# Kernel tuning notes

Measured on AMD Instinct MI355X. Metric: run time of the kernel, lower is better.

The kernel has to match this reference:

```python
import jax, jax.numpy as jnp
import numpy as np

LEAKY_ALPHA = 0.2  # LeakyReLU negative slope from init arg `alpha`


def setup_inputs() -> dict:
    key = jax.random.key(0)
    k1, k2, k3, k4 = jax.random.split(key, 4)
    B, N, Fin, Fout = 8, 2048, 256, 256
    h = jax.random.normal(k1, (B, N, Fin), dtype=jnp.float32)
    adj = jax.random.randint(k2, (N, N), 0, 2, dtype=jnp.int32)
    W = jax.random.normal(k3, (Fin, Fout), dtype=jnp.float32) * (1.414 * (6.0 / (Fin + Fout)) ** 0.5)
    a = jax.random.normal(k4, (2 * Fout, 1), dtype=jnp.float32) * (1.414 * (6.0 / (2 * Fout + 1)) ** 0.5)
    return {"h": h, "adj": adj, "W": W, "a": a}


def reference(h, adj, W, a):
    # h: (B, N, Fin), adj: (N, N) int {0,1}, W: (Fin, Fout), a: (2*Fout, 1)
    Fout = W.shape[1]
    Wh = jnp.einsum('bnf,fo->bno', h, W)            # (B, N, Fout)
    a1 = a[:Fout, 0]                                  # attends to target node i
    a2 = a[Fout:, 0]                                  # attends to source node j
    # a^T [Wh_i || Wh_j] == (Wh_i . a1) + (Wh_j . a2); LeakyReLU applied after, as in original
    s_i = Wh @ a1                                     # (B, N)
    s_j = Wh @ a2                                     # (B, N)
    e = jax.nn.leaky_relu(s_i[:, :, None] + s_j[:, None, :], negative_slope=LEAKY_ALPHA)  # (B, N, N)
    N = Wh.shape[1]
    mask = (adj > 0) | jnp.eye(N, dtype=bool)         # adjacency + self-loops
    e = jnp.where(mask[None, :, :], e, -jnp.inf)
    attention = jax.nn.softmax(e, axis=-1)            # dropout is identity in eval
    attention = jnp.nan_to_num(attention, nan=0.0)
    h_prime = jnp.einsum('bij,bjo->bio', attention, Wh)  # (B, N, Fout)
    return jax.nn.elu(h_prime)                        # concat=True -> ELU
```

## Files before the change

### kernel.cpp

```cpp
#include <hip/hip_runtime.h>

typedef unsigned short u16;
typedef unsigned int   u32;
typedef unsigned long long u64;

typedef __bf16 bf16x8 __attribute__((ext_vector_type(8)));
typedef float  f32x4  __attribute__((ext_vector_type(4)));

#define MFMA_BF16(a,b,c) __builtin_amdgcn_mfma_f32_16x16x32_bf16((a),(b),(c),0,0,0)

__device__ __forceinline__ float bf2f(u16 u) {
    return __uint_as_float(((u32)u) << 16);
}
__device__ __forceinline__ u16 f2bf(float x) {
    u32 u = __float_as_uint(x);
    u += 0x7fffu + ((u >> 16) & 1u);
    return (u16)(u >> 16);
}
__device__ __forceinline__ float ldany(const void* p, size_t i, int f32) {
    return f32 ? ((const float*)p)[i] : bf2f(((const u16*)p)[i]);
}
__device__ __forceinline__ int detect_f32(const u32* hw) {
    u32 w = hw[threadIdx.x & 63];
    int e = (w >> 23) & 0xFF;
    u64 m = __ballot(e >= 64 && e <= 190);
    return __popcll(m) >= 32 ? 1 : 0;
}

__global__ __launch_bounds__(256) void kprep(const void* __restrict__ w, const void* __restrict__ a,
                                             const int* __restrict__ adj,
                                             u16* __restrict__ wt, float* __restrict__ wa1,
                                             float* __restrict__ wa2, u64* __restrict__ mb64,
                                             int* __restrict__ cnt, const u32* __restrict__ hw) {
    __shared__ float s1[4], s2[4];
    int bid = blockIdx.x, t = threadIdx.x;
    int wid = t >> 6, lane = t & 63;
    if (bid < 256) {
        if (bid == 0 && t < 8) cnt[t] = 0;
        int f32 = detect_f32(hw);
        int k = bid, o = t;
        float wv = ldany(w, (size_t)k * 256 + o, f32);
        wt[o * 256 + k] = f2bf(wv);
        float p1 = wv * ldany(a, o, f32);
        float p2 = wv * ldany(a, 256 + o, f32);
        for (int d = 32; d; d >>= 1) { p1 += __shfl_down(p1, d); p2 += __shfl_down(p2, d); }
        if (lane == 0) { s1[wid] = p1; s2[wid] = p2; }
        __syncthreads();
        if (o == 0) { wa1[k] = s1[0] + s1[1] + s1[2] + s1[3]; wa2[k] = s2[0] + s2[1] + s2[2] + s2[3]; }
    } else {
        int w2 = (bid - 256) * 4 + wid;
        int4 v[2]; int rowv[2], jbv[2];
        #pragma unroll
        for (int s = 0; s < 2; s++) {
            int task = w2 * 2 + s;
            int row = task >> 3, jb = (task & 7) * 256;
            rowv[s] = row; jbv[s] = jb;
            v[s] = *(const int4*)(adj + (size_t)row * 2048 + jb + lane * 4);
        }
        #pragma unroll
        for (int s = 0; s < 2; s++) {
            int row = rowv[s], jb = jbv[s];
            int j0 = jb + lane * 4;
            u32 nib = (u32)(v[s].x > 0 || j0     == row)
                    | ((u32)(v[s].y > 0 || j0 + 1 == row) << 1)
                    | ((u32)(v[s].z > 0 || j0 + 2 == row) << 2)
                    | ((u32)(v[s].w > 0 || j0 + 3 == row) << 3);
            u32 sh = 4 * (lane & 7);
            u32 lo = (lane & 8) ? 0u : (nib << sh);
            u32 hi = (lane & 8) ? (nib << sh) : 0u;
            #pragma unroll
            for (int d = 1; d <= 8; d <<= 1) {
                lo |= __shfl_xor(lo, d);
                hi |= __shfl_xor(hi, d);
            }
            if ((lane & 15) == 0)
                mb64[(size_t)row * 32 + (jb >> 6) + (lane >> 4)] =
                    (u64)lo | ((u64)hi << 32);
        }
    }
}

struct __align__(16) K2LDS {
    u16 At[64 * 68];
    union { u16 Bt[256 * 68]; u16 Ct[256 * 68]; };
    float wa1s[256], wa2s[256];
    float s1[64], s2[64];
};
__global__ __launch_bounds__(1024, 4) void k2(const void* __restrict__ h, const u16* __restrict__ wt,
                                              const float* __restrict__ wa1, const float* __restrict__ wa2,
                                              u16* __restrict__ whbt,
                                              float* __restrict__ sig, float* __restrict__ sjg) {
    __shared__ K2LDS L;
    int f32 = detect_f32((const u32*)h);
    int m0 = blockIdx.x * 64;
    int b  = m0 >> 11;
    int n0 = m0 & 2047;
    int t = threadIdx.x;
    int wid = t >> 6, lane = t & 63, ln = lane & 15, qd = lane >> 4;

    if (t < 256) { L.wa1s[t] = wa1[t]; L.wa2s[t] = wa2[t]; }
    if (t < 64) { L.s1[t] = 0.f; L.s2[t] = 0.f; }
    __syncthreads();

    float a1 = 0.f, a2 = 0.f;
    f32x4 acc[4];
    for (int mi = 0; mi < 4; mi++) acc[mi] = (f32x4){0.f, 0.f, 0.f, 0.f};

    for (int c = 0; c < 4; c++) {
        int k0c = c * 64;
        if (t < 512) {
            int r = t >> 3, s = t & 7;
            float xv[8]; u16 uv[8];
            if (f32) {
                const float* src = (const float*)h + (size_t)(m0 + r) * 256 + k0c + s * 8;
                f32x4 x0 = *(const f32x4*)src;
                f32x4 x1 = *(const f32x4*)(src + 4);
                #pragma unroll
                for (int q = 0; q < 4; q++) { xv[q] = x0[q]; xv[4 + q] = x1[q]; }
                #pragma unroll
                for (int q = 0; q < 8; q++) uv[q] = f2bf(xv[q]);
            } else {
                const u16* src = (const u16*)h + (size_t)(m0 + r) * 256 + k0c + s * 8;
                *(uint4*)uv = *(const uint4*)src;
                #pragma unroll
                for (int q = 0; q < 8; q++) xv[q] = bf2f(uv[q]);
            }
            *(uint4*)&L.At[r * 68 + s * 8] = *(uint4*)uv;
            float pa = 0.f, pb = 0.f;
            #pragma unroll
            for (int q = 0; q < 8; q++) {
                pa += xv[q] * L.wa1s[k0c + s * 8 + q];
                pb += xv[q] * L.wa2s[k0c + s * 8 + q];
            }
            a1 += pa; a2 += pb;
        } else {
            int tt = t - 512;
            #pragma unroll
            for (int p = 0; p < 4; p++) {
                int f = (tt >> 3) + p * 64, s = tt & 7;
                *(uint4*)&L.Bt[f * 68 + s * 8] =
                    *(const uint4*)(wt + (size_t)f * 256 + k0c + s * 8);
            }
        }
        __syncthreads();
        for (int ks = 0; ks < 2; ks++) {
            bf16x8 af[4], bfr;
            for (int mi = 0; mi < 4; mi++)
                af[mi] = *(const bf16x8*)&L.At[(mi * 16 + ln) * 68 + ks * 32 + qd * 8];
            bfr = *(const bf16x8*)&L.Bt[(wid * 16 + ln) * 68 + ks * 32 + qd * 8];
            for (int mi = 0; mi < 4; mi++)
                acc[mi] = MFMA_BF16(af[mi], bfr, acc[mi]);
        }
        __syncthreads();
    }

    if (t < 512) {
        atomicAdd(&L.s1[t >> 3], a1);
        atomicAdd(&L.s2[t >> 3], a2);
    }
    for (int mi = 0; mi < 4; mi++) {
        int f = wid * 16 + ln;
        int n = mi * 16 + qd * 4;
        u16 v[4];
        for (int r = 0; r < 4; r++) v[r] = f2bf(acc[mi][r]);
        *(uint2*)&L.Ct[f * 68 + n] = *(uint2*)v;
    }
    __syncthreads();
    if (t < 64) { sig[m0 + t] = L.s1[t]; sjg[m0 + t] = L.s2[t]; }
    {
        int fr = t >> 2, q0 = (t & 3) * 2;
        size_t base = (size_t)b * 524288 + (size_t)fr * 2048 + n0;
        #pragma unroll
        for (int k = 0; k < 2; k++) {
            int s = q0 + k;
            uint4 v = *(uint4*)&L.Ct[fr * 68 + s * 8];
            *(uint4*)(whbt + base + s * 8) = v;
        }
    }
}

struct __align__(16) K4LDS {
    u32   vpack[2048];
    u16   sjb[2048];
    u64   mw[64 * 33];
    float u1[64], u2[64], nsi[64], inv[64];
    float lred[1024];
    u16   Pt[2][8192];
    int   claim[2];
};
__global__ __launch_bounds__(1024, 4) void k4(const float* __restrict__ sig,
                                              const float* __restrict__ sjg,
                                              const u64* __restrict__ mb64, const u16* __restrict__ whbt,
                                              void* __restrict__ out, const void* __restrict__ hdet,
                                              int* __restrict__ cnt) {
    __shared__ K4LDS L;
    int f32 = detect_f32((const u32*)hdet);
    int t = threadIdx.x;
    if (t == 0) {
        int xcd = __builtin_amdgcn_s_getreg(63508) & 7;
        int bsel = 0, tile = 0;
        #pragma unroll
        for (int k = 0; k < 8; k++) {
            int bb = (xcd + k) & 7;
            int tt = atomicAdd(&cnt[bb], 1);
            if (tt < 32) { bsel = bb; tile = tt; break; }
        }
        L.claim[0] = bsel; L.claim[1] = tile;
    }
    __syncthreads();
    int b  = L.claim[0];
    int i0 = L.claim[1] * 64;
    int wid = t >> 6, lane = t & 63, ln = lane & 15, qd = lane >> 4;
    const u16* wb = whbt + (size_t)b * 524288 + (size_t)wid * 16 * 2048;
    float lacc = 0.f;

    bf16x8 br[2][4];
    #define LOAD_B(cc, bb) do {                                             \
        int j0_ = (cc) * 128;                                               \
        _Pragma("unroll")                                                   \
        for (int ks = 0; ks < 4; ks++)                                      \
            br[bb][ks] = *(const bf16x8*)(wb +                              \
                (size_t)ln * 2048 + j0_ + ks * 32 + qd * 8);                \
    } while (0)

    #define PGEN(cc, bb) do {                                               \
        int r_ = t & 63, o_ = t >> 6;                                       \
        int jb_ = (cc) * 128 + o_ * 8;                                      \
        uint4 pkA_ = *(const uint4*)&L.vpack[jb_];                          \
        uint4 pkB_ = *(const uint4*)&L.vpack[jb_ + 4];                      \
        uint4 sj4_ = *(const uint4*)&L.sjb[jb_];                            \
        u32 mb_ = (u32)(L.mw[r_ * 33 + 2 * (cc) + (o_ >> 3)]                \
                        >> ((o_ & 7) * 8)) & 0xffu;                         \
        float u1_ = L.u1[r_], u2_ = L.u2[r_], nsi_ = L.nsi[r_];             \
        u32 pr_[4];                                                         \
        _Pragma("unroll")                                                   \
        for (int pk = 0; pk < 4; pk++) {                                    \
            u32 vw0_ = (pk == 0) ? pkA_.x : (pk == 1) ? pkA_.z              \
                     : (pk == 2) ? pkB_.x : pkB_.z;                         \
            u32 vw1_ = (pk == 0) ? pkA_.y : (pk == 1) ? pkA_.w              \
                     : (pk == 2) ? pkB_.y : pkB_.w;                         \
            u32 sw_ = (pk == 0) ? sj4_.x : (pk == 1) ? sj4_.y               \
                     : (pk == 2) ? sj4_.z : sj4_.w;                         \
            float sj0_ = __uint_as_float(sw_ << 16);                        \
            float sj1_ = __uint_as_float(sw_ & 0xffff0000u);                \
            float p0_, p1_;                                                 \
            {                                                               \
                bool pos = sj0_ > nsi_;                                     \
                float vv = __uint_as_float(pos ? (vw0_ << 16)               \
                                               : ((vw0_ >> 16) << 16));     \
                p0_ = (pos ? u1_ : u2_) * vv;                               \
                p0_ = ((mb_ >> (2 * pk)) & 1u) ? p0_ : 0.f;                 \
            }                                                               \
            {                                                               \
                bool pos = sj1_ > nsi_;                                     \
                float vv = __uint_as_float(pos ? (vw1_ << 16)               \
                                               : ((vw1_ >> 16) << 16));     \
                p1_ = (pos ? u1_ : u2_) * vv;                               \
                p1_ = ((mb_ >> (2 * pk + 1)) & 1u) ? p1_ : 0.f;             \
            }                                                               \
            lacc += p0_ + p1_;                                              \
            pr_[pk] = __builtin_amdgcn_perm(__float_as_uint(p1_),           \
                                            __float_as_uint(p0_),           \
                                            0x07060302u);                   \
        }                                                                   \
        *(uint4*)&L.Pt[bb][t * 8] = *(uint4*)pr_;                           \
    } while (0)

    LOAD_B(0, 0);
    float sjv0 = sjg[b * 2048 + t];
    float sjv1 = sjg[b * 2048 + 1024 + t];
    {
        float mx = fmaxf(sjv0, sjv1);
        for (int d = 32; d; d >>= 1) mx = fmaxf(mx, __shfl_xor(mx, d));
        if (lane == 0) L.lred[wid] = mx;
    }
    for (int p = 0; p < 2; p++) {
        int idx = t + p * 1024;
        int r = idx >> 5, c = idx & 31;
        L.mw[r * 33 + c] = mb64[(size_t)(i0 + r) * 32 + c];
    }
    __syncthreads();
    float Mb;
    {
        float m0_ = fmaxf(fmaxf(fmaxf(L.lred[0], L.lred[1]), fmaxf(L.lred[2], L.lred[3])),
                          fmaxf(fmaxf(L.lred[4], L.lred[5]), fmaxf(L.lred[6], L.lred[7])));
        float m1_ = fmaxf(fmaxf(fmaxf(L.lred[8], L.lred[9]), fmaxf(L.lred[10], L.lred[11])),
                          fmaxf(fmaxf(L.lred[12], L.lred[13]), fmaxf(L.lred[14], L.lred[15])));
        Mb = fmaxf(m0_, m1_);
    }
    {
        float vj0 = __expf(sjv0 - Mb), v2j0 = __expf(0.2f * (sjv0 - Mb));
        L.vpack[t] = (u32)f2bf(vj0) | ((u32)f2bf(v2j0) << 16);
        L.sjb[t] = f2bf(sjv0);
        float vj1 = __expf(sjv1 - Mb), v2j1 = __expf(0.2f * (sjv1 - Mb));
        L.vpack[t + 1024] = (u32)f2bf(vj1) | ((u32)f2bf(v2j1) << 16);
        L.sjb[t + 1024] = f2bf(sjv1);
    }
    if (t < 64) {
        float siv = sig[b * 2048 + i0 + t];
        float x = siv + Mb;
        float K = fmaxf(x, 0.2f * x);
        L.u1[t] = __expf(x - K);
        L.u2[t] = __expf(0.2f * x - K);
        L.nsi[t] = -siv;
    }
    __syncthreads();
    PGEN(0, 0);

    f32x4 acc[4];
    for (int mi = 0; mi < 4; mi++)
        acc[mi] = (f32x4){0.f, 0.f, 0.f, 0.f};

    #define STEP(c, cur, nxt) do {                                          \
        __syncthreads();                                                    \
        if ((c) < 15) { LOAD_B((c) + 1, nxt); PGEN((c) + 1, nxt); }         \
        __builtin_amdgcn_s_setprio(1);                                      \
        _Pragma("unroll")                                                   \
        for (int ks = 0; ks < 4; ks++) {                                    \
            bf16x8 af[4];                                                   \
            _Pragma("unroll")                                               \
            for (int mi = 0; mi < 4; mi++)                                  \
                af[mi] = *(const bf16x8*)&L.Pt[cur][((ks * 4 + qd) * 64 +   \
                                                     mi * 16 + ln) * 8];    \
            _Pragma("unroll")                                               \
            for (int mi = 0; mi < 4; mi++)                                  \
                acc[mi] = MFMA_BF16(af[mi], br[cur][ks], acc[mi]);          \
        }                                                                   \
        __builtin_amdgcn_s_setprio(0);                                      \
    } while (0)

    for (int cc = 0; cc < 8; cc++) {
        STEP(2 * cc,     0, 1);
        STEP(2 * cc + 1, 1, 0);
    }

    __syncthreads();
    L.lred[t] = lacc;
    __syncthreads();
    if (t < 64) {
        float s = 0.f;
        #pragma unroll
        for (int q = 0; q < 16; q++) s += L.lred[q * 64 + t];
        L.inv[t] = 1.0f / s;
    }
    __syncthreads();

    {
        int fg = wid * 16 + ln;
        for (int mi = 0; mi < 4; mi++) {
            for (int reg = 0; reg < 4; reg++) {
                int rl = mi * 16 + qd * 4 + reg;
                float hp = acc[mi][reg] * L.inv[rl];
                float y = hp > 0.f ? hp : (__expf(hp) - 1.f);
                size_t idx = (size_t)(b * 2048 + i0 + rl) * 256 + fg;
                if (f32) ((float*)out)[idx] = y;
                else     ((u16*)out)[idx]   = f2bf(y);
            }
        }
    }
    #undef LOAD_B
    #undef PGEN
    #undef STEP
}

extern "C" void kernel_launch(void* const* d_in, const int* in_sizes, int n_in,
                              void* d_out, int out_size, void* d_ws, size_t ws_size,
                              hipStream_t stream) {
    const void* h   = d_in[0];
    const int*  adj = (const int*)d_in[1];
    const void* W   = d_in[2];
    const void* a   = d_in[3];

    char* ws = (char*)d_ws;
    u16*   WT    = (u16*)  (ws + 0);
    float* si    = (float*)(ws + 131072);
    float* sj    = (float*)(ws + 196608);
    u64*   mb64  = (u64*)  (ws + 557056);
    u16*   whbt  = (u16*)  (ws + 1081344);
    float* Wa1   = (float*)(ws + 9469952);
    float* Wa2   = (float*)(ws + 9470976);
    int*   cnt   = (int*)  (ws + 9472000);

    kprep<<<dim3(2304), dim3(256),  0, stream>>>(W, a, adj, WT, Wa1, Wa2, mb64, cnt, (const u32*)h);
    k2   <<<dim3(256),  dim3(1024), 0, stream>>>(h, WT, Wa1, Wa2, whbt, si, sj);
    k4   <<<dim3(256),  dim3(1024), 0, stream>>>(si, sj, mb64, whbt, d_out, h, cnt);
}
```

Baseline: 130.7 us.

## Fuse weight prep and adjacency packing into projection kernel, dropping one launch

Merges the prep kernel (W transpose/bf16 conversion, W·a reductions, adjacency bitmask packing) into the projection kernel, so there are two launches instead of three. Each projection block now recomputes W·a1 and W·a2 locally and reads W rows directly, converting them to bf16 in LDS. The MFMA B fragments are then gathered with scalar strided LDS reads instead of one vector load. This removes one launch and the transposed-W workspace round trip, but adds redundant W reads and reductions in every block plus slower, bank-conflict-prone B fragment loads.

```diff
diff --git a/kernel.cpp b/kernel.cpp
--- a/kernel.cpp
+++ b/kernel.cpp
@@ -27,28 +27,25 @@
     return __popcll(m) >= 32 ? 1 : 0;
 }
 
-__global__ __launch_bounds__(256) void kprep(const void* __restrict__ w, const void* __restrict__ a,
-                                             const int* __restrict__ adj,
-                                             u16* __restrict__ wt, float* __restrict__ wa1,
-                                             float* __restrict__ wa2, u64* __restrict__ mb64,
-                                             int* __restrict__ cnt, const u32* __restrict__ hw) {
-    __shared__ float s1[4], s2[4];
+struct __align__(16) KFLDS {
+    u16 At[64 * 68];
+    union { u16 Wrow[64 * 258]; u16 Ct[256 * 68]; };
+    float asA[512];
+    float wa1s[256], wa2s[256];
+    float s1[64], s2[64];
+};
+__global__ __launch_bounds__(1024, 4) void kfront(
+        const void* __restrict__ h, const int* __restrict__ adj,
+        const void* __restrict__ w, const void* __restrict__ a,
+        u16* __restrict__ whbt, float* __restrict__ sig, float* __restrict__ sjg,
+        u64* __restrict__ mb64, int* __restrict__ cnt) {
+    __shared__ KFLDS L;
     int bid = blockIdx.x, t = threadIdx.x;
-    int wid = t >> 6, lane = t & 63;
-    if (bid < 256) {
-        if (bid == 0 && t < 8) cnt[t] = 0;
-        int f32 = detect_f32(hw);
-        int k = bid, o = t;
-        float wv = ldany(w, (size_t)k * 256 + o, f32);
-        wt[o * 256 + k] = f2bf(wv);
-        float p1 = wv * ldany(a, o, f32);
-        float p2 = wv * ldany(a, 256 + o, f32);
-        for (int d = 32; d; d >>= 1) { p1 += __shfl_down(p1, d); p2 += __shfl_down(p2, d); }
-        if (lane == 0) { s1[wid] = p1; s2[wid] = p2; }
-        __syncthreads();
-        if (o == 0) { wa1[k] = s1[0] + s1[1] + s1[2] + s1[3]; wa2[k] = s2[0] + s2[1] + s2[2] + s2[3]; }
-    } else {
-        int w2 = (bid - 256) * 4 + wid;
+    int wid = t >> 6, lane = t & 63, ln = lane & 15, qd = lane >> 4;
+
+    if (bid >= 256) {
+        if (bid == 256 && t < 8) cnt[t] = 0;
+        int w2 = (bid - 256) * 16 + wid;
         int4 v[2]; int rowv[2], jbv[2];
         #pragma unroll
         for (int s = 0; s < 2; s++) {
@@ -77,29 +74,50 @@
                 mb64[(size_t)row * 32 + (jb >> 6) + (lane >> 4)] =
                     (u64)lo | ((u64)hi << 32);
         }
-    }
-}
-
-struct __align__(16) K2LDS {
-    u16 At[64 * 68];
-    union { u16 Bt[256 * 68]; u16 Ct[256 * 68]; };
-    float wa1s[256], wa2s[256];
-    float s1[64], s2[64];
-};
-__global__ __launch_bounds__(1024, 4) void k2(const void* __restrict__ h, const u16* __restrict__ wt,
-                                              const float* __restrict__ wa1, const float* __restrict__ wa2,
-                                              u16* __restrict__ whbt,
-                                              float* __restrict__ sig, float* __restrict__ sjg) {
-    __shared__ K2LDS L;
+        return;
+    }
+
     int f32 = detect_f32((const u32*)h);
-    int m0 = blockIdx.x * 64;
+    int m0 = bid * 64;
     int b  = m0 >> 11;
     int n0 = m0 & 2047;
-    int t = threadIdx.x;
-    int wid = t >> 6, lane = t & 63, ln = lane & 15, qd = lane >> 4;
-
-    if (t < 256) { L.wa1s[t] = wa1[t]; L.wa2s[t] = wa2[t]; }
+
+    if (t < 512) L.asA[t] = ldany(a, t, f32);
+    if (t < 256) { L.wa1s[t] = 0.f; L.wa2s[t] = 0.f; }
     if (t < 64) { L.s1[t] = 0.f; L.s2[t] = 0.f; }
+    __syncthreads();
+
+    {
+        int r = t >> 2, o0 = (t & 3) * 64;
+        float pa = 0.f, pb = 0.f;
+        if (f32) {
+            const float* wp = (const float*)w + (size_t)r * 256 + o0;
+            #pragma unroll
+            for (int q = 0; q < 64; q += 4) {
+                f32x4 x = *(const f32x4*)(wp + q);
+                #pragma unroll
+                for (int q2 = 0; q2 < 4; q2++) {
+                    pa += x[q2] * L.asA[o0 + q + q2];
+                    pb += x[q2] * L.asA[256 + o0 + q + q2];
+                }
+            }
+        } else {
+            const u16* wp = (const u16*)w + (size_t)r * 256 + o0;
+            #pragma unroll
+            for (int q = 0; q < 64; q += 8) {
+                u16 uv[8];
+                *(uint4*)uv = *(const uint4*)(wp + q);
+                #pragma unroll
+                for (int q2 = 0; q2 < 8; q2++) {
+                    float wv = bf2f(uv[q2]);
+                    pa += wv * L.asA[o0 + q + q2];
+                    pb += wv * L.asA[256 + o0 + q + q2];
+                }
+            }
+        }
+        atomicAdd(&L.wa1s[r], pa);
+        atomicAdd(&L.wa2s[r], pb);
+    }
     __syncthreads();
 
     float a1 = 0.f, a2 = 0.f;
@@ -135,19 +153,36 @@
             a1 += pa; a2 += pb;
         } else {
             int tt = t - 512;
-            #pragma unroll
-            for (int p = 0; p < 4; p++) {
-                int f = (tt >> 3) + p * 64, s = tt & 7;
-                *(uint4*)&L.Bt[f * 68 + s * 8] =
-                    *(const uint4*)(wt + (size_t)f * 256 + k0c + s * 8);
-            }
+            int rl = tt >> 3, s = tt & 7, o0 = s * 32;
+            u16 wv16[32];
+            if (f32) {
+                const float* src = (const float*)w + (size_t)(k0c + rl) * 256 + o0;
+                #pragma unroll
+                for (int i = 0; i < 32; i += 4) {
+                    f32x4 x = *(const f32x4*)(src + i);
+                    #pragma unroll
+                    for (int q2 = 0; q2 < 4; q2++) wv16[i + q2] = f2bf(x[q2]);
+                }
+            } else {
+                const u16* src = (const u16*)w + (size_t)(k0c + rl) * 256 + o0;
+                #pragma unroll
+                for (int i = 0; i < 32; i += 8)
+                    *(uint4*)&wv16[i] = *(const uint4*)(src + i);
+            }
+            u32* wr32 = (u32*)&L.Wrow[rl * 258 + o0];
+            #pragma unroll
+            for (int i = 0; i < 16; i++) wr32[i] = *(u32*)&wv16[2 * i];
         }
         __syncthreads();
         for (int ks = 0; ks < 2; ks++) {
             bf16x8 af[4], bfr;
             for (int mi = 0; mi < 4; mi++)
                 af[mi] = *(const bf16x8*)&L.At[(mi * 16 + ln) * 68 + ks * 32 + qd * 8];
-            bfr = *(const bf16x8*)&L.Bt[(wid * 16 + ln) * 68 + ks * 32 + qd * 8];
+            u16 tmp[8];
+            #pragma unroll
+            for (int q = 0; q < 8; q++)
+                tmp[q] = L.Wrow[(ks * 32 + qd * 8 + q) * 258 + wid * 16 + ln];
+            bfr = *(const bf16x8*)tmp;
             for (int mi = 0; mi < 4; mi++)
                 acc[mi] = MFMA_BF16(af[mi], bfr, acc[mi]);
         }
@@ -372,16 +407,12 @@
     const void* a   = d_in[3];
 
     char* ws = (char*)d_ws;
-    u16*   WT    = (u16*)  (ws + 0);
     float* si    = (float*)(ws + 131072);
     float* sj    = (float*)(ws + 196608);
     u64*   mb64  = (u64*)  (ws + 557056);
     u16*   whbt  = (u16*)  (ws + 1081344);
-    float* Wa1   = (float*)(ws + 9469952);
-    float* Wa2   = (float*)(ws + 9470976);
     int*   cnt   = (int*)  (ws + 9472000);
 
-    kprep<<<dim3(2304), dim3(256),  0, stream>>>(W, a, adj, WT, Wa1, Wa2, mb64, cnt, (const u32*)h);
-    k2   <<<dim3(256),  dim3(1024), 0, stream>>>(h, WT, Wa1, Wa2, whbt, si, sj);
-    k4   <<<dim3(256),  dim3(1024), 0, stream>>>(si, sj, mb64, whbt, d_out, h, cnt);
-}
+    kfront<<<dim3(768), dim3(1024), 0, stream>>>(h, adj, W, a, whbt, si, sj, mb64, cnt);
+    k4    <<<dim3(256), dim3(1024), 0, stream>>>(si, sj, mb64, whbt, d_out, h, cnt);
+}
```

Measured after the change: 146.0 us. 1.12x slower.
